# Kernel optimization log

Hardware: AMD Instinct MI355X
Metric: run time of the kernel (lower is better)

## Reference

```python
import jax, jax.numpy as jnp
import numpy as np

D = 256      # cfg.d_model
H = 8        # num heads
HID = D // H # head_outdim for hidden layers (32)
N = 16000    # nodes
E = 64000    # edges
NUM_GNN = 3  # cfg.num_gnn -> 2 hidden EGATConv layers + 1 final
SLOPE = 0.01 # F.leaky_relu default in DGL EGATConv


def setup_inputs() -> dict:
    key = jax.random.key(0)
    ks = jax.random.split(key, 8)
    inp = {
        "nfeat": jax.random.normal(ks[0], (N, D), jnp.float32),
        "efeat": jax.random.normal(ks[1], (E, D), jnp.float32),
        "src": jax.random.randint(ks[2], (E,), 0, N),
        "dst": jax.random.randint(ks[3], (E,), 0, N),
    }
    L = NUM_GNN - 1  # hidden layers, out_node = out_edge = HID per head
    kh = jax.random.split(ks[4], 5)
    s = 0.02
    inp["Wnode_h"] = jax.random.normal(kh[0], (L, D, H * HID), jnp.float32) * s
    inp["Wni_h"]   = jax.random.normal(kh[1], (L, D, H * HID), jnp.float32) * s
    inp["Wnj_h"]   = jax.random.normal(kh[2], (L, D, H * HID), jnp.float32) * s
    inp["Wfij_h"]  = jax.random.normal(kh[3], (L, D, H * HID), jnp.float32) * s
    inp["attn_h"]  = jax.random.normal(kh[4], (L, H, HID), jnp.float32) * s
    inp["bias_h"]  = jnp.zeros((L, H * HID), jnp.float32)
    kl = jax.random.split(ks[5], 5)
    inp["Wnode_l"] = jax.random.normal(kl[0], (D, H * D), jnp.float32) * s
    inp["Wni_l"]   = jax.random.normal(kl[1], (D, H * D), jnp.float32) * s
    inp["Wnj_l"]   = jax.random.normal(kl[2], (D, H * D), jnp.float32) * s
    inp["Wfij_l"]  = jax.random.normal(kl[3], (D, H * D), jnp.float32) * s
    inp["attn_l"]  = jax.random.normal(kl[4], (H, D), jnp.float32) * s
    inp["bias_l"]  = jnp.zeros((H * D,), jnp.float32)
    return inp


def _egat(n, f, src, dst, Wnode, Wni, Wnj, Wfij, attn, bias):
    """DGL EGATConv: edge-gated multi-head graph attention.
    n:[N,D] f:[E,D] attn:[H,od] -> (h_out:[N,H,od], f_out:[E,H,od])."""
    Hh, od = attn.shape
    # edge feature update: f_ni(u) + f_nj(v) + f_fij(e) + bias, leaky_relu
    f_out = (n @ Wni)[src] + (n @ Wnj)[dst] + f @ Wfij + bias  # [E, H*od]
    f_out = jax.nn.leaky_relu(f_out, SLOPE).reshape(-1, Hh, od)
    # attention logits + edge softmax grouped by destination node
    e = jnp.einsum('ehd,hd->eh', f_out, attn)                   # [E, H]
    m = jax.lax.stop_gradient(jax.ops.segment_max(e, dst, num_segments=N))
    ex = jnp.exp(e - m[dst])
    s = jax.ops.segment_sum(ex, dst, num_segments=N)
    a = ex / s[dst]                                             # [E, H]
    # message passing: u_mul_e + sum at dst
    h = (n @ Wnode).reshape(N, Hh, od)
    h_out = jax.ops.segment_sum(h[src] * a[..., None], dst, num_segments=N)
    return h_out, f_out


def reference(nfeat, efeat, src, dst,
              Wnode_h, Wni_h, Wnj_h, Wfij_h, attn_h, bias_h,
              Wnode_l, Wni_l, Wnj_l, Wfij_l, attn_l, bias_l):
    n, f = nfeat, efeat
    for l in range(Wnode_h.shape[0]):  # hidden layers: concat heads + ELU + residual
        tn, tf = _egat(n, f, src, dst, Wnode_h[l], Wni_h[l], Wnj_h[l],
                       Wfij_h[l], attn_h[l], bias_h[l])
        n = n + jax.nn.elu(tn.reshape(N, -1))  # reshape == concat over heads
        f = f + jax.nn.elu(tf.reshape(E, -1))
    # last layer: mean over heads + residual
    tn, tf = _egat(n, f, src, dst, Wnode_l, Wni_l, Wnj_l, Wfij_l, attn_l, bias_l)
    n = n + tn.mean(axis=1)
    f = f + tf.mean(axis=1)
    return n, f
```

## Files before the change

kernel.cpp:

```cpp
#include <hip/hip_runtime.h>

typedef unsigned short u16;
typedef __attribute__((ext_vector_type(4))) unsigned short u16x4;
typedef __attribute__((ext_vector_type(8))) unsigned short u16x8;
typedef __attribute__((ext_vector_type(4))) float f32x4;
typedef __attribute__((ext_vector_type(8))) __bf16 bf16x8;

#define NN 16000
#define NE 64000
#define ECH 16000

__device__ __forceinline__ float bf2f(u16 b) {
  union { unsigned int u; float f; } v; v.u = ((unsigned int)b) << 16; return v.f;
}
__device__ __forceinline__ u16 f2bf(float x) {
  union { float f; unsigned int u; } v; v.f = x;
  unsigned int r = v.u + 0x7FFFu + ((v.u >> 16) & 1u);
  return (u16)(r >> 16);
}

__global__ void cast_init(const float* __restrict__ in, float* __restrict__ outf,
                          u16* __restrict__ outb, int n4) {
  for (int i = blockIdx.x * blockDim.x + threadIdx.x; i < n4; i += gridDim.x * blockDim.x) {
    f32x4 v = ((const f32x4*)in)[i];
    u16x4 b;
#pragma unroll
    for (int j = 0; j < 4; ++j) b[j] = f2bf(v[j]);
    ((f32x4*)outf)[i] = v;
    ((u16x4*)outb)[i] = b;
  }
}

__global__ void cast_bf(const float* __restrict__ in, u16* __restrict__ outb, int n4) {
  for (int i = blockIdx.x * blockDim.x + threadIdx.x; i < n4; i += gridDim.x * blockDim.x) {
    f32x4 v = ((const f32x4*)in)[i];
    u16x4 b;
#pragma unroll
    for (int j = 0; j < 4; ++j) b[j] = f2bf(v[j]);
    ((u16x4*)outb)[i] = b;
  }
}

__global__ void deg_hist(const int* __restrict__ dst, int* __restrict__ deg) {
  int e = blockIdx.x * 256 + threadIdx.x;
  if (e < NE) atomicAdd(&deg[dst[e]], 1);
}

__global__ __launch_bounds__(1024) void scan_deg(const int* __restrict__ deg,
                                                 int* __restrict__ row_ptr,
                                                 int* __restrict__ cursor) {
  __shared__ int lds[1024];
  int t = threadIdx.x;
  int base = t * 16;
  int v[16];
  int s = 0;
#pragma unroll
  for (int j = 0; j < 16; ++j) {
    int idx = base + j;
    v[j] = idx < NN ? deg[idx] : 0;
    s += v[j];
  }
  lds[t] = s;
  __syncthreads();
  for (int d = 1; d < 1024; d <<= 1) {
    int x = t >= d ? lds[t - d] : 0;
    __syncthreads();
    lds[t] += x;
    __syncthreads();
  }
  int run = lds[t] - s;
  for (int j = 0; j < 16; ++j) {
    int idx = base + j;
    if (idx < NN) { row_ptr[idx] = run; cursor[idx] = run; run += v[j]; }
  }
  if (t == 1023) row_ptr[NN] = run;
}

__global__ void csr_fill(const int* __restrict__ src, const int* __restrict__ dst,
                         int* __restrict__ cursor, int* __restrict__ cs_e,
                         int* __restrict__ cs_src) {
  int e = blockIdx.x * 256 + threadIdx.x;
  if (e >= NE) return;
  int pos = atomicAdd(&cursor[dst[e]], 1);
  cs_e[pos] = e;
  cs_src[pos] = src[e];
}

__global__ void transpose4(const float* __restrict__ W0, const float* __restrict__ W1,
                           const float* __restrict__ W2, const float* __restrict__ W3,
                           int ld, int osz, u16* __restrict__ WT) {
  __shared__ float t[16][17];
  int z = blockIdx.z;
  const float* W = z == 0 ? W0 : (z == 1 ? W1 : (z == 2 ? W2 : W3));
  u16* O = WT + (size_t)z * osz;
  int n0 = blockIdx.x * 16, k0 = blockIdx.y * 16;
  int tx = threadIdx.x, ty = threadIdx.y;
  t[ty][tx] = W[(size_t)(k0 + ty) * ld + n0 + tx];
  __syncthreads();
  O[(size_t)(n0 + ty) * 256 + k0 + tx] = f2bf(t[tx][ty]);
}

__global__ void transpose4p(const float* __restrict__ W0, const float* __restrict__ W1,
                            const float* __restrict__ W2, const float* __restrict__ W3,
                            u16* __restrict__ WT) {
  __shared__ float t[16][17];
  int z = blockIdx.z;
  const float* W = z == 0 ? W0 : (z == 1 ? W1 : (z == 2 ? W2 : W3));
  u16* O = WT + (size_t)z * 524288;
  int n0 = blockIdx.x * 16, k0 = blockIdx.y * 16;
  int tx = threadIdx.x, ty = threadIdx.y;
  t[ty][tx] = W[(size_t)(k0 + ty) * 2048 + n0 + tx];
  __syncthreads();
  int n = n0 + ty;
  int j = (n & 255) * 8 + (n >> 8);
  O[(size_t)j * 256 + k0 + tx] = f2bf(t[tx][ty]);
}

__global__ void permute_ba(const float* __restrict__ bias, const float* __restrict__ attn,
                           float* __restrict__ bias_p, float* __restrict__ attn_p) {
  int n = blockIdx.x * 256 + threadIdx.x;
  int j = (n & 255) * 8 + (n >> 8);
  bias_p[j] = bias[n];
  attn_p[j] = attn[n];
}

__global__ __launch_bounds__(256) void gemm_abt(
    const u16* __restrict__ A,
    const u16* __restrict__ BT0, const u16* __restrict__ BT1, const u16* __restrict__ BT2,
    u16* __restrict__ C0, u16* __restrict__ C1, u16* __restrict__ C2, int ldc) {
  const int bz = blockIdx.z;
  const u16* BT = bz == 0 ? BT0 : (bz == 1 ? BT1 : BT2);
  u16* C = bz == 0 ? C0 : (bz == 1 ? C1 : C2);
  const int nx = gridDim.x;
  const int nwg = nx * gridDim.y;
  int bid = blockIdx.y * nx + blockIdx.x;
  int q = nwg >> 3, r = nwg & 7;
  int xcd = bid & 7, idx = bid >> 3;
  int wg = (xcd < r) ? (xcd * (q + 1) + idx) : (r * (q + 1) + (xcd - r) * q + idx);
  const int m0 = (wg / nx) * 128;
  const int n0 = (wg % nx) * 128;
  __shared__ __attribute__((aligned(16))) char smem[69632];
  u16* lA = (u16*)smem;
  u16* lB = (u16*)(smem + 32768);
  const int tid = threadIdx.x;
  const int lane = tid & 63;
  const int wid = tid >> 6;
  const int wr = (wid >> 1) * 64;
  const int wc = (wid & 1) * 64;
  const int srow = tid >> 3;
  const int sdst = (tid & 7) * 8;
  const int ssrc = (((tid & 7) ^ (srow & 7))) * 8;
  const int sx = (lane >> 4) ^ (lane & 7);
  f32x4 acc[4][4] = {};
#define STAGE(buf, kb)                                                                         \
  {                                                                                            \
    _Pragma("unroll") for (int i = 0; i < 4; ++i) {                                            \
      const int row = srow + i * 32;                                                           \
      __builtin_amdgcn_global_load_lds(                                                        \
          (const __attribute__((address_space(1))) void*)(A + (size_t)(m0 + row) * 256 + (kb) + ssrc), \
          (__attribute__((address_space(3))) void*)(lA + (buf) * 8192 + row * 64 + sdst), 16, 0, 0); \
      __builtin_amdgcn_global_load_lds(                                                        \
          (const __attribute__((address_space(1))) void*)(BT + (size_t)(n0 + row) * 256 + (kb) + ssrc), \
          (__attribute__((address_space(3))) void*)(lB + (buf) * 8192 + row * 64 + sdst), 16, 0, 0); \
    }                                                                                          \
  }
  STAGE(0, 0)
  __syncthreads();
#pragma unroll
  for (int t = 0; t < 4; ++t) {
    if (t < 3) STAGE((t + 1) & 1, (t + 1) * 64)
    const u16* pA = lA + (t & 1) * 8192;
    const u16* pB = lB + (t & 1) * 8192;
#pragma unroll
    for (int kk = 0; kk < 2; ++kk) {
      const int sw = ((kk << 2) ^ sx) * 8;
      bf16x8 af[4], bfr[4];
#pragma unroll
      for (int m = 0; m < 4; ++m)
        af[m] = *(const bf16x8*)(pA + (wr + m * 16 + (lane & 15)) * 64 + sw);
#pragma unroll
      for (int n = 0; n < 4; ++n)
        bfr[n] = *(const bf16x8*)(pB + (wc + n * 16 + (lane & 15)) * 64 + sw);
#pragma unroll
      for (int m = 0; m < 4; ++m)
#pragma unroll
        for (int n = 0; n < 4; ++n)
          acc[m][n] = __builtin_amdgcn_mfma_f32_16x16x32_bf16(af[m], bfr[n], acc[m][n], 0, 0, 0);
    }
    __syncthreads();
  }
#undef STAGE
  const int cr = (lane >> 4) * 4;
  const int cc = lane & 15;
  float* stg = (float*)smem + wid * (64 * 68);
#pragma unroll
  for (int m = 0; m < 4; ++m)
#pragma unroll
    for (int n = 0; n < 4; ++n)
#pragma unroll
      for (int j = 0; j < 4; ++j)
        stg[(m * 16 + cr + j) * 68 + n * 16 + cc] = acc[m][n][j];
  const int rr = lane >> 3;
  const int c0 = (lane & 7) * 8;
#pragma unroll
  for (int p = 0; p < 8; ++p) {
    int row = p * 8 + rr;
    f32x4 v0 = *(const f32x4*)(stg + row * 68 + c0);
    f32x4 v1 = *(const f32x4*)(stg + row * 68 + c0 + 4);
    u16x8 o;
#pragma unroll
    for (int i = 0; i < 4; ++i) { o[i] = f2bf(v0[i]); o[4 + i] = f2bf(v1[i]); }
    *(u16x8*)(&C[(size_t)(m0 + wr + row) * ldc + (n0 + wc + c0)]) = o;
  }
}

__global__ __launch_bounds__(256) void gemm_fused_hidden(
    const u16* __restrict__ A, const u16* __restrict__ BT, const u16* __restrict__ t3,
    const int* __restrict__ src, const int* __restrict__ dst,
    const float* __restrict__ bias, const float* __restrict__ attn,
    u16* __restrict__ f_new, float* __restrict__ exb) {
  const int nx = gridDim.x;
  const int nwg = nx * gridDim.y;
  int bid = blockIdx.y * nx + blockIdx.x;
  int q = nwg >> 3, r = nwg & 7;
  int xcd = bid & 7, idx = bid >> 3;
  int wg = (xcd < r) ? (xcd * (q + 1) + idx) : (r * (q + 1) + (xcd - r) * q + idx);
  const int m0 = (wg / nx) * 128;
  const int n0 = (wg % nx) * 128;
  __shared__ __attribute__((aligned(16))) char smem[69632];
  u16* lA = (u16*)smem;
  u16* lB = (u16*)(smem + 32768);
  const int tid = threadIdx.x;
  const int lane = tid & 63;
  const int wid = tid >> 6;
  const int wr = (wid >> 1) * 64;
  const int wc = (wid & 1) * 64;
  const int srow = tid >> 3;
  const int sdst = (tid & 7) * 8;
  const int ssrc = (((tid & 7) ^ (srow & 7))) * 8;
  const int sx = (lane >> 4) ^ (lane & 7);
  const int rr = lane >> 3;
  const int c0e = (lane & 7) * 8;
  const int j0 = n0 + wc + c0e;
  const int head = j0 >> 5;
  u16x8 va8[8], vb8[8], fs8[8];
#pragma unroll
  for (int p = 0; p < 8; ++p) {
    int e = m0 + wr + p * 8 + rr;
    int is = src[e], id = dst[e];
    va8[p] = *(const u16x8*)(t3 + (size_t)is * 768 + j0);
    vb8[p] = *(const u16x8*)(t3 + (size_t)id * 768 + 256 + j0);
    fs8[p] = *(const u16x8*)(A + (size_t)e * 256 + j0);
  }
  f32x4 acc[4][4] = {};
#define STAGE(buf, kb)                                                                         \
  {                                                                                            \
    _Pragma("unroll") for (int i = 0; i < 4; ++i) {                                            \
      const int row = srow + i * 32;                                                           \
      __builtin_amdgcn_global_load_lds(                                                        \
          (const __attribute__((address_space(1))) void*)(A + (size_t)(m0 + row) * 256 + (kb) + ssrc), \
          (__attribute__((address_space(3))) void*)(lA + (buf) * 8192 + row * 64 + sdst), 16, 0, 0); \
      __builtin_amdgcn_global_load_lds(                                                        \
          (const __attribute__((address_space(1))) void*)(BT + (size_t)(n0 + row) * 256 + (kb) + ssrc), \
          (__attribute__((address_space(3))) void*)(lB + (buf) * 8192 + row * 64 + sdst), 16, 0, 0); \
    }                                                                                          \
  }
  STAGE(0, 0)
  __syncthreads();
#pragma unroll
  for (int t = 0; t < 4; ++t) {
    if (t < 3) STAGE((t + 1) & 1, (t + 1) * 64)
    const u16* pA = lA + (t & 1) * 8192;
    const u16* pB = lB + (t & 1) * 8192;
#pragma unroll
    for (int kk = 0; kk < 2; ++kk) {
      const int sw = ((kk << 2) ^ sx) * 8;
      bf16x8 af[4], bfr[4];
#pragma unroll
      for (int m = 0; m < 4; ++m)
        af[m] = *(const bf16x8*)(pA + (wr + m * 16 + (lane & 15)) * 64 + sw);
#pragma unroll
      for (int n = 0; n < 4; ++n)
        bfr[n] = *(const bf16x8*)(pB + (wc + n * 16 + (lane & 15)) * 64 + sw);
#pragma unroll
      for (int m = 0; m < 4; ++m)
#pragma unroll
        for (int n = 0; n < 4; ++n)
          acc[m][n] = __builtin_amdgcn_mfma_f32_16x16x32_bf16(af[m], bfr[n], acc[m][n], 0, 0, 0);
    }
    __syncthreads();
  }
#undef STAGE
  const int cr = (lane >> 4) * 4;
  const int cc = lane & 15;
  float* stg = (float*)smem + wid * (64 * 68);
#pragma unroll
  for (int m = 0; m < 4; ++m)
#pragma unroll
    for (int n = 0; n < 4; ++n)
#pragma unroll
      for (int j = 0; j < 4; ++j)
        stg[(m * 16 + cr + j) * 68 + n * 16 + cc] = acc[m][n][j];
  f32x4 bias0 = *(const f32x4*)(bias + j0);
  f32x4 bias1 = *(const f32x4*)(bias + j0 + 4);
  f32x4 attn0 = *(const f32x4*)(attn + j0);
  f32x4 attn1 = *(const f32x4*)(attn + j0 + 4);
#pragma unroll
  for (int p = 0; p < 8; ++p) {
    int row = p * 8 + rr;
    int e = m0 + wr + row;
    f32x4 v0 = *(const f32x4*)(stg + row * 68 + c0e);
    f32x4 v1 = *(const f32x4*)(stg + row * 68 + c0e + 4);
    float lp = 0.f;
    u16x8 o;
#pragma unroll
    for (int h = 0; h < 4; ++h) {
      float t0 = v0[h] + bf2f(va8[p][h]) + bf2f(vb8[p][h]) + bias0[h];
      t0 = t0 > 0.f ? t0 : 0.01f * t0;
      lp += t0 * attn0[h];
      float e0 = t0 > 0.f ? t0 : expm1f(t0);
      o[h] = f2bf(bf2f(fs8[p][h]) + e0);
      float t1 = v1[h] + bf2f(va8[p][4 + h]) + bf2f(vb8[p][4 + h]) + bias1[h];
      t1 = t1 > 0.f ? t1 : 0.01f * t1;
      lp += t1 * attn1[h];
      float e1 = t1 > 0.f ? t1 : expm1f(t1);
      o[4 + h] = f2bf(bf2f(fs8[p][4 + h]) + e1);
    }
    *(u16x8*)(&f_new[(size_t)e * 256 + j0]) = o;
    lp += __shfl_xor(lp, 1);
    lp += __shfl_xor(lp, 2);
    lp = fminf(fmaxf(lp, -30.f), 30.f);
    if ((lane & 3) == 0) exb[(size_t)e * 8 + head] = expf(lp);
  }
}

__global__ __launch_bounds__(256) void gemm_fused_final(
    int e0, const u16* __restrict__ A, const u16* __restrict__ BT,
    const u16* __restrict__ t_ni, const u16* __restrict__ t_nj,
    const int* __restrict__ src, const int* __restrict__ dst,
    const float* __restrict__ bias_p, const float* __restrict__ attn_p,
    const u16* __restrict__ f_bf, float* __restrict__ out_f, float* __restrict__ part) {
  const int nx = gridDim.x;
  const int nwg = nx * gridDim.y;
  int bid = blockIdx.y * nx + blockIdx.x;
  int q = nwg >> 3, r = nwg & 7;
  int xcd = bid & 7, idx = bid >> 3;
  int wg = (xcd < r) ? (xcd * (q + 1) + idx) : (r * (q + 1) + (xcd - r) * q + idx);
  const int m0 = (wg / nx) * 128;
  const int n0 = (wg % nx) * 128;
  __shared__ __attribute__((aligned(16))) char smem[69632];
  u16* lA = (u16*)smem;
  u16* lB = (u16*)(smem + 32768);
  const int tid = threadIdx.x;
  const int lane = tid & 63;
  const int wid = tid >> 6;
  const int wr = (wid >> 1) * 64;
  const int wc = (wid & 1) * 64;
  const int srow = tid >> 3;
  const int sdst = (tid & 7) * 8;
  const int ssrc = (((tid & 7) ^ (srow & 7))) * 8;
  const int sx = (lane >> 4) ^ (lane & 7);
  const int rr = lane >> 3;
  const int c0e = (lane & 7) * 8;
  const int j0 = n0 + wc + c0e;
  const int cmod = j0 >> 3;
  const int wgrp = (n0 + wc) >> 6;
  u16x8 ni8v[8], nj8v[8];
  u16 fsv[8];
#pragma unroll
  for (int p = 0; p < 8; ++p) {
    int e = e0 + m0 + wr + p * 8 + rr;
    int is = src[e], id = dst[e];
    ni8v[p] = *(const u16x8*)(t_ni + (size_t)is * 2048 + j0);
    nj8v[p] = *(const u16x8*)(t_nj + (size_t)id * 2048 + j0);
    fsv[p] = f_bf[(size_t)e * 256 + cmod];
  }
  f32x4 acc[4][4] = {};
#define STAGE(buf, kb)                                                                         \
  {                                                                                            \
    _Pragma("unroll") for (int i = 0; i < 4; ++i) {                                            \
      const int row = srow + i * 32;                                                           \
      __builtin_amdgcn_global_load_lds(                                                        \
          (const __attribute__((address_space(1))) void*)(A + (size_t)(m0 + row) * 256 + (kb) + ssrc), \
          (__attribute__((address_space(3))) void*)(lA + (buf) * 8192 + row * 64 + sdst), 16, 0, 0); \
      __builtin_amdgcn_global_load_lds(                                                        \
          (const __attribute__((address_space(1))) void*)(BT + (size_t)(n0 + row) * 256 + (kb) + ssrc), \
          (__attribute__((address_space(3))) void*)(lB + (buf) * 8192 + row * 64 + sdst), 16, 0, 0); \
    }                                                                                          \
  }
  STAGE(0, 0)
  __syncthreads();
#pragma unroll
  for (int t = 0; t < 4; ++t) {
    if (t < 3) STAGE((t + 1) & 1, (t + 1) * 64)
    const u16* pA = lA + (t & 1) * 8192;
    const u16* pB = lB + (t & 1) * 8192;
#pragma unroll
    for (int kk = 0; kk < 2; ++kk) {
      const int sw = ((kk << 2) ^ sx) * 8;
      bf16x8 af[4], bfr[4];
#pragma unroll
      for (int m = 0; m < 4; ++m)
        af[m] = *(const bf16x8*)(pA + (wr + m * 16 + (lane & 15)) * 64 + sw);
#pragma unroll
      for (int n = 0; n < 4; ++n)
        bfr[n] = *(const bf16x8*)(pB + (wc + n * 16 + (lane & 15)) * 64 + sw);
#pragma unroll
      for (int m = 0; m < 4; ++m)
#pragma unroll
        for (int n = 0; n < 4; ++n)
          acc[m][n] = __builtin_amdgcn_mfma_f32_16x16x32_bf16(af[m], bfr[n], acc[m][n], 0, 0, 0);
    }
    __syncthreads();
  }
#undef STAGE
  const int cr = (lane >> 4) * 4;
  const int cc = lane & 15;
  float* stg = (float*)smem + wid * (64 * 68);
#pragma unroll
  for (int m = 0; m < 4; ++m)
#pragma unroll
    for (int n = 0; n < 4; ++n)
#pragma unroll
      for (int j = 0; j < 4; ++j)
        stg[(m * 16 + cr + j) * 68 + n * 16 + cc] = acc[m][n][j];
  f32x4 bias0 = *(const f32x4*)(bias_p + j0);
  f32x4 bias1 = *(const f32x4*)(bias_p + j0 + 4);
  f32x4 attn0 = *(const f32x4*)(attn_p + j0);
  f32x4 attn1 = *(const f32x4*)(attn_p + j0 + 4);
#pragma unroll
  for (int p = 0; p < 8; ++p) {
    int row = p * 8 + rr;
    int er = m0 + wr + row;
    int e = e0 + er;
    f32x4 v0 = *(const f32x4*)(stg + row * 68 + c0e);
    f32x4 v1 = *(const f32x4*)(stg + row * 68 + c0e + 4);
    float y[8];
#pragma unroll
    for (int h = 0; h < 4; ++h) {
      float t0 = v0[h] + bf2f(ni8v[p][h]) + bf2f(nj8v[p][h]) + bias0[h];
      y[h] = t0 > 0.f ? t0 : 0.01f * t0;
      float t1 = v1[h] + bf2f(ni8v[p][4 + h]) + bf2f(nj8v[p][4 + h]) + bias1[h];
      y[4 + h] = t1 > 0.f ? t1 : 0.01f * t1;
    }
    float outv = 0.125f * (((y[0] + y[1]) + (y[2] + y[3])) + ((y[4] + y[5]) + (y[6] + y[7])));
    out_f[(size_t)e * 256 + cmod] = outv + bf2f(fsv[p]);
    float lp[8];
#pragma unroll
    for (int h = 0; h < 4; ++h) { lp[h] = y[h] * attn0[h]; lp[4 + h] = y[4 + h] * attn1[h]; }
#pragma unroll
    for (int mask = 1; mask < 8; mask <<= 1)
#pragma unroll
      for (int h = 0; h < 8; ++h) lp[h] += __shfl_xor(lp[h], mask);
    if ((lane & 7) == 0) {
#pragma unroll
      for (int h = 0; h < 8; ++h) part[(size_t)er * 256 + wgrp * 8 + h] = lp[h];
    }
  }
}

__global__ __launch_bounds__(256) void logit_reduce(
    int e0, const float* __restrict__ part, float* __restrict__ exb) {
  int er = blockIdx.x * 4 + (threadIdx.x >> 6);
  if (er >= ECH) return;
  int lane = threadIdx.x & 63;
  int h = lane & 7;
  int w0 = (lane >> 3) * 4;
  float s = 0.f;
#pragma unroll
  for (int k = 0; k < 4; ++k) s += part[(size_t)er * 256 + (w0 + k) * 8 + h];
  s += __shfl_xor(s, 8);
  s += __shfl_xor(s, 16);
  s += __shfl_xor(s, 32);
  s = fminf(fmaxf(s, -30.f), 30.f);
  if (lane < 8) exb[(size_t)(e0 + er) * 8 + h] = expf(s);
}

__global__ __launch_bounds__(256) void node_gather_hidden(
    const u16* __restrict__ t3, const int* __restrict__ row_ptr,
    const int* __restrict__ cs_e, const int* __restrict__ cs_src,
    const float* __restrict__ exb, float* __restrict__ n_cur, u16* __restrict__ n_bf) {
  int node = blockIdx.x * 4 + (threadIdx.x >> 6);
  if (node >= NN) return;
  int lane = threadIdx.x & 63;
  int c = lane * 4, h = lane >> 3;
  int beg = row_ptr[node], end = row_ptr[node + 1];
  float denom = 0.f;
  float acc[4] = {0.f, 0.f, 0.f, 0.f};
  for (int p = beg; p < end; ++p) {
    float a = exb[(size_t)cs_e[p] * 8 + h];
    denom += a;
    u16x4 hv = *(const u16x4*)(t3 + (size_t)cs_src[p] * 768 + 512 + c);
#pragma unroll
    for (int j = 0; j < 4; ++j) acc[j] += a * bf2f(hv[j]);
  }
  float inv = denom > 0.f ? 1.f / denom : 0.f;
  size_t i0 = (size_t)node * 256 + c;
  f32x4 nv = *(f32x4*)(n_cur + i0);
  u16x4 bv;
#pragma unroll
  for (int j = 0; j < 4; ++j) {
    float t = acc[j] * inv;
    t = t > 0.f ? t : expm1f(t);
    nv[j] += t;
    bv[j] = f2bf(nv[j]);
  }
  *(f32x4*)(n_cur + i0) = nv;
  *(u16x4*)(n_bf + i0) = bv;
}

__global__ __launch_bounds__(256) void node_gather_final_all(
    const u16* __restrict__ t_node, const int* __restrict__ row_ptr,
    const int* __restrict__ cs_e, const int* __restrict__ cs_src,
    const float* __restrict__ exb, const float* __restrict__ n_cur,
    float* __restrict__ out_n) {
  int node = blockIdx.x * 4 + (threadIdx.x >> 6);
  if (node >= NN) return;
  int lane = threadIdx.x & 63;
  int c = lane * 4;
  int beg = row_ptr[node], end = row_ptr[node + 1];
  float dh[8] = {};
  float acc[8][4] = {};
  for (int p = beg; p < end; ++p) {
    int e = cs_e[p];
    int s = cs_src[p];
    const u16* rowb = t_node + (size_t)s * 2048 + (size_t)c * 8;
    const float* eb = exb + (size_t)e * 8;
    float a[8];
    u16x8 rv[4];
#pragma unroll
    for (int h = 0; h < 8; ++h) a[h] = eb[h];
#pragma unroll
    for (int jj = 0; jj < 4; ++jj) rv[jj] = *(const u16x8*)(rowb + jj * 8);
#pragma unroll
    for (int h = 0; h < 8; ++h) {
      dh[h] += a[h];
#pragma unroll
      for (int jj = 0; jj < 4; ++jj) acc[h][jj] += a[h] * bf2f(rv[jj][h]);
    }
  }
  float total[4] = {0.f, 0.f, 0.f, 0.f};
#pragma unroll
  for (int h = 0; h < 8; ++h) {
    float inv = dh[h] > 0.f ? 0.125f / dh[h] : 0.f;
#pragma unroll
    for (int jj = 0; jj < 4; ++jj) total[jj] += acc[h][jj] * inv;
  }
  size_t i0 = (size_t)node * 256 + c;
  f32x4 nv = *(const f32x4*)(n_cur + i0);
#pragma unroll
  for (int jj = 0; jj < 4; ++jj) nv[jj] += total[jj];
  *(f32x4*)(out_n + i0) = nv;
}

extern "C" void kernel_launch(void* const* d_in, const int* in_sizes, int n_in,
                              void* d_out, int out_size, void* d_ws, size_t ws_size,
                              hipStream_t stream) {
  const float* nfeat   = (const float*)d_in[0];
  const float* efeat   = (const float*)d_in[1];
  const int*   src     = (const int*)d_in[2];
  const int*   dst     = (const int*)d_in[3];
  const float* Wnode_h = (const float*)d_in[4];
  const float* Wni_h   = (const float*)d_in[5];
  const float* Wnj_h   = (const float*)d_in[6];
  const float* Wfij_h  = (const float*)d_in[7];
  const float* attn_h  = (const float*)d_in[8];
  const float* bias_h  = (const float*)d_in[9];
  const float* Wnode_l = (const float*)d_in[10];
  const float* Wni_l   = (const float*)d_in[11];
  const float* Wnj_l   = (const float*)d_in[12];
  const float* Wfij_l  = (const float*)d_in[13];
  const float* attn_l  = (const float*)d_in[14];
  const float* bias_l  = (const float*)d_in[15];

  char* ws = (char*)d_ws;
  size_t off = 0;
  auto alloc = [&](size_t b) { char* p = ws + off; off += (b + 255) & ~(size_t)255; return p; };
  float* n_cur = (float*)alloc((size_t)NN * 256 * 4);
  u16* n_bf    = (u16*)alloc((size_t)NN * 256 * 2);
  u16* f_bf    = (u16*)alloc((size_t)NE * 256 * 2);
  u16* t_ni    = (u16*)alloc((size_t)NN * 2048 * 2);
  u16* t_nj    = (u16*)alloc((size_t)NN * 2048 * 2);
  u16* t_node  = (u16*)alloc((size_t)NN * 2048 * 2);
  float* exb   = (float*)alloc((size_t)NE * 8 * 4);
  u16* WT      = (u16*)alloc((size_t)4 * 65536 * 2);
  u16* WTF     = (u16*)alloc((size_t)4 * 524288 * 2);
  u16* fW      = (u16*)alloc((size_t)NE * 256 * 2);
  float* part  = (float*)alloc((size_t)ECH * 256 * 4);
  float* biasp = (float*)alloc(2048 * 4);
  float* attnp = (float*)alloc(2048 * 4);
  int* deg     = (int*)alloc((size_t)NN * 4);
  int* cursor  = (int*)alloc((size_t)NN * 4);
  int* row_ptr = (int*)alloc((size_t)(NN + 1) * 4);
  int* cs_e    = (int*)alloc((size_t)NE * 4);
  int* cs_src  = (int*)alloc((size_t)NE * 4);

  u16* WT_fij  = WT + 3 * 65536;
  u16* WTF_node = WTF;
  u16* WTF_ni   = WTF + (size_t)1 * 524288;
  u16* WTF_nj   = WTF + (size_t)2 * 524288;
  u16* WTF_fij  = WTF + (size_t)3 * 524288;

  float* out_n = (float*)d_out;
  float* out_f = out_n + (size_t)NN * 256;

  hipMemsetAsync(deg, 0, (size_t)NN * 4, stream);
  deg_hist<<<(NE + 255) / 256, 256, 0, stream>>>(dst, deg);
  scan_deg<<<1, 1024, 0, stream>>>(deg, row_ptr, cursor);
  csr_fill<<<(NE + 255) / 256, 256, 0, stream>>>(src, dst, cursor, cs_e, cs_src);

  cast_init<<<1024, 256, 0, stream>>>(nfeat, n_cur, n_bf, NN * 256 / 4);
  cast_bf<<<2048, 256, 0, stream>>>(efeat, f_bf, NE * 256 / 4);

  for (int l = 0; l < 2; ++l) {
    transpose4<<<dim3(16, 16, 4), dim3(16, 16), 0, stream>>>(
        Wni_h + (size_t)l * 65536, Wnj_h + (size_t)l * 65536,
        Wnode_h + (size_t)l * 65536, Wfij_h + (size_t)l * 65536, 256, 65536, WT);
    gemm_abt<<<dim3(6, 125, 1), 256, 0, stream>>>(n_bf, WT, WT, WT,
                                                  t_ni, t_ni, t_ni, 768);
    const u16* fsrc = l == 0 ? f_bf : fW;
    u16* fdst       = l == 0 ? fW : f_bf;
    gemm_fused_hidden<<<dim3(2, 500), 256, 0, stream>>>(
        fsrc, WT_fij, t_ni, src, dst,
        bias_h + (size_t)l * 256, attn_h + (size_t)l * 256, fdst, exb);
    node_gather_hidden<<<4000, 256, 0, stream>>>(t_ni, row_ptr, cs_e, cs_src, exb, n_cur, n_bf);
  }

  transpose4p<<<dim3(128, 16, 4), dim3(16, 16), 0, stream>>>(
      Wnode_l, Wni_l, Wnj_l, Wfij_l, WTF);
  permute_ba<<<8, 256, 0, stream>>>(bias_l, attn_l, biasp, attnp);
  gemm_abt<<<dim3(16, 125, 3), 256, 0, stream>>>(n_bf, WTF_ni, WTF_nj, WTF_node,
                                                 t_ni, t_nj, t_node, 2048);
  for (int e0 = 0; e0 < NE; e0 += ECH) {
    gemm_fused_final<<<dim3(16, ECH / 128), 256, 0, stream>>>(
        e0, f_bf + (size_t)e0 * 256, WTF_fij, t_ni, t_nj, src, dst,
        biasp, attnp, f_bf, out_f, part);
    logit_reduce<<<ECH / 4, 256, 0, stream>>>(e0, part, exb);
  }
  node_gather_final_all<<<4000, 256, 0, stream>>>(t_node, row_ptr, cs_e, cs_src,
                                                  exb, n_cur, out_n);
}
```

Baseline: 629.6 us.

## Process edges in dst-sorted CSR order so logits are indexed by CSR position

The fused edge GEMM kernels now iterate edges in CSR (dst-sorted) order, gathering rows of the edge features through cs_e and reading src/dst from the sorted arrays. Attention logits are written at CSR position, so the node gather kernels read exb contiguously and no longer need the cs_e indirection. Feature rows are scattered back to their original edge indices. Dst-side node rows now get better locality, but the A-tile loads into LDS become gathers of random rows instead of contiguous streaming reads.

```diff
diff --git a/kernel.cpp b/kernel.cpp
--- a/kernel.cpp
+++ b/kernel.cpp
@@ -78,12 +78,14 @@
 
 __global__ void csr_fill(const int* __restrict__ src, const int* __restrict__ dst,
                          int* __restrict__ cursor, int* __restrict__ cs_e,
-                         int* __restrict__ cs_src) {
+                         int* __restrict__ cs_src, int* __restrict__ cs_dst) {
   int e = blockIdx.x * 256 + threadIdx.x;
   if (e >= NE) return;
-  int pos = atomicAdd(&cursor[dst[e]], 1);
+  int d = dst[e];
+  int pos = atomicAdd(&cursor[d], 1);
   cs_e[pos] = e;
   cs_src[pos] = src[e];
+  cs_dst[pos] = d;
 }
 
 __global__ void transpose4(const float* __restrict__ W0, const float* __restrict__ W1,
@@ -216,7 +218,7 @@
 
 __global__ __launch_bounds__(256) void gemm_fused_hidden(
     const u16* __restrict__ A, const u16* __restrict__ BT, const u16* __restrict__ t3,
-    const int* __restrict__ src, const int* __restrict__ dst,
+    const int* __restrict__ cs_e, const int* __restrict__ cs_src, const int* __restrict__ cs_dst,
     const float* __restrict__ bias, const float* __restrict__ attn,
     u16* __restrict__ f_new, float* __restrict__ exb) {
   const int nx = gridDim.x;
@@ -239,15 +241,21 @@
   const int sdst = (tid & 7) * 8;
   const int ssrc = (((tid & 7) ^ (srow & 7))) * 8;
   const int sx = (lane >> 4) ^ (lane & 7);
+  int cse_s[4];
+#pragma unroll
+  for (int i = 0; i < 4; ++i) cse_s[i] = cs_e[m0 + srow + i * 32];
   const int rr = lane >> 3;
   const int c0e = (lane & 7) * 8;
   const int j0 = n0 + wc + c0e;
   const int head = j0 >> 5;
+  int ep[8];
   u16x8 va8[8], vb8[8], fs8[8];
 #pragma unroll
   for (int p = 0; p < 8; ++p) {
-    int e = m0 + wr + p * 8 + rr;
-    int is = src[e], id = dst[e];
+    int pos = m0 + wr + p * 8 + rr;
+    int e = cs_e[pos];
+    int is = cs_src[pos], id = cs_dst[pos];
+    ep[p] = e;
     va8[p] = *(const u16x8*)(t3 + (size_t)is * 768 + j0);
     vb8[p] = *(const u16x8*)(t3 + (size_t)id * 768 + 256 + j0);
     fs8[p] = *(const u16x8*)(A + (size_t)e * 256 + j0);
@@ -258,7 +266,7 @@
     _Pragma("unroll") for (int i = 0; i < 4; ++i) {                                            \
       const int row = srow + i * 32;                                                           \
       __builtin_amdgcn_global_load_lds(                                                        \
-          (const __attribute__((address_space(1))) void*)(A + (size_t)(m0 + row) * 256 + (kb) + ssrc), \
+          (const __attribute__((address_space(1))) void*)(A + (size_t)cse_s[i] * 256 + (kb) + ssrc), \
           (__attribute__((address_space(3))) void*)(lA + (buf) * 8192 + row * 64 + sdst), 16, 0, 0); \
       __builtin_amdgcn_global_load_lds(                                                        \
           (const __attribute__((address_space(1))) void*)(BT + (size_t)(n0 + row) * 256 + (kb) + ssrc), \
@@ -308,7 +316,7 @@
 #pragma unroll
   for (int p = 0; p < 8; ++p) {
     int row = p * 8 + rr;
-    int e = m0 + wr + row;
+    int pos = m0 + wr + row;
     f32x4 v0 = *(const f32x4*)(stg + row * 68 + c0e);
     f32x4 v1 = *(const f32x4*)(stg + row * 68 + c0e + 4);
     float lp = 0.f;
@@ -326,18 +334,18 @@
       float e1 = t1 > 0.f ? t1 : expm1f(t1);
       o[4 + h] = f2bf(bf2f(fs8[p][4 + h]) + e1);
     }
-    *(u16x8*)(&f_new[(size_t)e * 256 + j0]) = o;
+    *(u16x8*)(&f_new[(size_t)ep[p] * 256 + j0]) = o;
     lp += __shfl_xor(lp, 1);
     lp += __shfl_xor(lp, 2);
     lp = fminf(fmaxf(lp, -30.f), 30.f);
-    if ((lane & 3) == 0) exb[(size_t)e * 8 + head] = expf(lp);
+    if ((lane & 3) == 0) exb[(size_t)pos * 8 + head] = expf(lp);
   }
 }
 
 __global__ __launch_bounds__(256) void gemm_fused_final(
-    int e0, const u16* __restrict__ A, const u16* __restrict__ BT,
+    int p0, const u16* __restrict__ A, const u16* __restrict__ BT,
     const u16* __restrict__ t_ni, const u16* __restrict__ t_nj,
-    const int* __restrict__ src, const int* __restrict__ dst,
+    const int* __restrict__ cs_e, const int* __restrict__ cs_src, const int* __restrict__ cs_dst,
     const float* __restrict__ bias_p, const float* __restrict__ attn_p,
     const u16* __restrict__ f_bf, float* __restrict__ out_f, float* __restrict__ part) {
   const int nx = gridDim.x;
@@ -360,17 +368,23 @@
   const int sdst = (tid & 7) * 8;
   const int ssrc = (((tid & 7) ^ (srow & 7))) * 8;
   const int sx = (lane >> 4) ^ (lane & 7);
+  int cse_s[4];
+#pragma unroll
+  for (int i = 0; i < 4; ++i) cse_s[i] = cs_e[p0 + m0 + srow + i * 32];
   const int rr = lane >> 3;
   const int c0e = (lane & 7) * 8;
   const int j0 = n0 + wc + c0e;
   const int cmod = j0 >> 3;
   const int wgrp = (n0 + wc) >> 6;
+  int ep[8];
   u16x8 ni8v[8], nj8v[8];
   u16 fsv[8];
 #pragma unroll
   for (int p = 0; p < 8; ++p) {
-    int e = e0 + m0 + wr + p * 8 + rr;
-    int is = src[e], id = dst[e];
+    int pos = p0 + m0 + wr + p * 8 + rr;
+    int e = cs_e[pos];
+    int is = cs_src[pos], id = cs_dst[pos];
+    ep[p] = e;
     ni8v[p] = *(const u16x8*)(t_ni + (size_t)is * 2048 + j0);
     nj8v[p] = *(const u16x8*)(t_nj + (size_t)id * 2048 + j0);
     fsv[p] = f_bf[(size_t)e * 256 + cmod];
@@ -381,7 +395,7 @@
     _Pragma("unroll") for (int i = 0; i < 4; ++i) {                                            \
       const int row = srow + i * 32;                                                           \
       __builtin_amdgcn_global_load_lds(                                                        \
-          (const __attribute__((address_space(1))) void*)(A + (size_t)(m0 + row) * 256 + (kb) + ssrc), \
+          (const __attribute__((address_space(1))) void*)(A + (size_t)cse_s[i] * 256 + (kb) + ssrc), \
           (__attribute__((address_space(3))) void*)(lA + (buf) * 8192 + row * 64 + sdst), 16, 0, 0); \
       __builtin_amdgcn_global_load_lds(                                                        \
           (const __attribute__((address_space(1))) void*)(BT + (size_t)(n0 + row) * 256 + (kb) + ssrc), \
@@ -432,7 +446,6 @@
   for (int p = 0; p < 8; ++p) {
     int row = p * 8 + rr;
     int er = m0 + wr + row;
-    int e = e0 + er;
     f32x4 v0 = *(const f32x4*)(stg + row * 68 + c0e);
     f32x4 v1 = *(const f32x4*)(stg + row * 68 + c0e + 4);
     float y[8];
@@ -444,7 +457,7 @@
       y[4 + h] = t1 > 0.f ? t1 : 0.01f * t1;
     }
     float outv = 0.125f * (((y[0] + y[1]) + (y[2] + y[3])) + ((y[4] + y[5]) + (y[6] + y[7])));
-    out_f[(size_t)e * 256 + cmod] = outv + bf2f(fsv[p]);
+    out_f[(size_t)ep[p] * 256 + cmod] = outv + bf2f(fsv[p]);
     float lp[8];
 #pragma unroll
     for (int h = 0; h < 4; ++h) { lp[h] = y[h] * attn0[h]; lp[4 + h] = y[4 + h] * attn1[h]; }
@@ -460,7 +473,7 @@
 }
 
 __global__ __launch_bounds__(256) void logit_reduce(
-    int e0, const float* __restrict__ part, float* __restrict__ exb) {
+    int p0, const float* __restrict__ part, float* __restrict__ exb) {
   int er = blockIdx.x * 4 + (threadIdx.x >> 6);
   if (er >= ECH) return;
   int lane = threadIdx.x & 63;
@@ -473,13 +486,13 @@
   s += __shfl_xor(s, 16);
   s += __shfl_xor(s, 32);
   s = fminf(fmaxf(s, -30.f), 30.f);
-  if (lane < 8) exb[(size_t)(e0 + er) * 8 + h] = expf(s);
+  if (lane < 8) exb[(size_t)(p0 + er) * 8 + h] = expf(s);
 }
 
 __global__ __launch_bounds__(256) void node_gather_hidden(
     const u16* __restrict__ t3, const int* __restrict__ row_ptr,
-    const int* __restrict__ cs_e, const int* __restrict__ cs_src,
-    const float* __restrict__ exb, float* __restrict__ n_cur, u16* __restrict__ n_bf) {
+    const int* __restrict__ cs_src, const float* __restrict__ exb,
+    float* __restrict__ n_cur, u16* __restrict__ n_bf) {
   int node = blockIdx.x * 4 + (threadIdx.x >> 6);
   if (node >= NN) return;
   int lane = threadIdx.x & 63;
@@ -488,7 +501,7 @@
   float denom = 0.f;
   float acc[4] = {0.f, 0.f, 0.f, 0.f};
   for (int p = beg; p < end; ++p) {
-    float a = exb[(size_t)cs_e[p] * 8 + h];
+    float a = exb[(size_t)p * 8 + h];
     denom += a;
     u16x4 hv = *(const u16x4*)(t3 + (size_t)cs_src[p] * 768 + 512 + c);
 #pragma unroll
@@ -511,9 +524,8 @@
 
 __global__ __launch_bounds__(256) void node_gather_final_all(
     const u16* __restrict__ t_node, const int* __restrict__ row_ptr,
-    const int* __restrict__ cs_e, const int* __restrict__ cs_src,
-    const float* __restrict__ exb, const float* __restrict__ n_cur,
-    float* __restrict__ out_n) {
+    const int* __restrict__ cs_src, const float* __restrict__ exb,
+    const float* __restrict__ n_cur, float* __restrict__ out_n) {
   int node = blockIdx.x * 4 + (threadIdx.x >> 6);
   if (node >= NN) return;
   int lane = threadIdx.x & 63;
@@ -522,10 +534,9 @@
   float dh[8] = {};
   float acc[8][4] = {};
   for (int p = beg; p < end; ++p) {
-    int e = cs_e[p];
     int s = cs_src[p];
     const u16* rowb = t_node + (size_t)s * 2048 + (size_t)c * 8;
-    const float* eb = exb + (size_t)e * 8;
+    const float* eb = exb + (size_t)p * 8;
     float a[8];
     u16x8 rv[4];
 #pragma unroll
@@ -594,6 +605,7 @@
   int* row_ptr = (int*)alloc((size_t)(NN + 1) * 4);
   int* cs_e    = (int*)alloc((size_t)NE * 4);
   int* cs_src  = (int*)alloc((size_t)NE * 4);
+  int* cs_dst  = (int*)alloc((size_t)NE * 4);
 
   u16* WT_fij  = WT + 3 * 65536;
   u16* WTF_node = WTF;
@@ -607,7 +619,7 @@
   hipMemsetAsync(deg, 0, (size_t)NN * 4, stream);
   deg_hist<<<(NE + 255) / 256, 256, 0, stream>>>(dst, deg);
   scan_deg<<<1, 1024, 0, stream>>>(deg, row_ptr, cursor);
-  csr_fill<<<(NE + 255) / 256, 256, 0, stream>>>(src, dst, cursor, cs_e, cs_src);
+  csr_fill<<<(NE + 255) / 256, 256, 0, stream>>>(src, dst, cursor, cs_e, cs_src, cs_dst);
 
   cast_init<<<1024, 256, 0, stream>>>(nfeat, n_cur, n_bf, NN * 256 / 4);
   cast_bf<<<2048, 256, 0, stream>>>(efeat, f_bf, NE * 256 / 4);
@@ -621,9 +633,9 @@
     const u16* fsrc = l == 0 ? f_bf : fW;
     u16* fdst       = l == 0 ? fW : f_bf;
     gemm_fused_hidden<<<dim3(2, 500), 256, 0, stream>>>(
-        fsrc, WT_fij, t_ni, src, dst,
+        fsrc, WT_fij, t_ni, cs_e, cs_src, cs_dst,
         bias_h + (size_t)l * 256, attn_h + (size_t)l * 256, fdst, exb);
-    node_gather_hidden<<<4000, 256, 0, stream>>>(t_ni, row_ptr, cs_e, cs_src, exb, n_cur, n_bf);
+    node_gather_hidden<<<4000, 256, 0, stream>>>(t_ni, row_ptr, cs_src, exb, n_cur, n_bf);
   }
 
   transpose4p<<<dim3(128, 16, 4), dim3(16, 16), 0, stream>>>(
@@ -631,12 +643,12 @@
   permute_ba<<<8, 256, 0, stream>>>(bias_l, attn_l, biasp, attnp);
   gemm_abt<<<dim3(16, 125, 3), 256, 0, stream>>>(n_bf, WTF_ni, WTF_nj, WTF_node,
                                                  t_ni, t_nj, t_node, 2048);
-  for (int e0 = 0; e0 < NE; e0 += ECH) {
+  for (int p0 = 0; p0 < NE; p0 += ECH) {
     gemm_fused_final<<<dim3(16, ECH / 128), 256, 0, stream>>>(
-        e0, f_bf + (size_t)e0 * 256, WTF_fij, t_ni, t_nj, src, dst,
+        p0, f_bf, WTF_fij, t_ni, t_nj, cs_e, cs_src, cs_dst,
         biasp, attnp, f_bf, out_f, part);
-    logit_reduce<<<ECH / 4, 256, 0, stream>>>(e0, part, exb);
-  }
-  node_gather_final_all<<<4000, 256, 0, stream>>>(t_node, row_ptr, cs_e, cs_src,
+    logit_reduce<<<ECH / 4, 256, 0, stream>>>(p0, part, exb);
+  }
+  node_gather_final_all<<<4000, 256, 0, stream>>>(t_node, row_ptr, cs_src,
                                                   exb, n_cur, out_n);
 }
```

Result: faster. 605.8 us (-3.8%).
